# Kernel tuning notes

Measured on AMD Instinct MI355X. Metric: run time of the kernel, lower is better.

Reference implementation:

```python
import jax, jax.numpy as jnp
import numpy as np

B, N, D = 4096, 64, 128
H = 2
M = 3 * D            # model_dim = feat + edge + time
DK = M // H          # d_k = d_v = 192


def setup_inputs() -> dict:
    key = jax.random.key(0)
    ks = jax.random.split(key, 20)
    s = 0.02
    mask = jax.random.randint(ks[6], (B, N), 0, 2).astype(bool)
    mask = mask.at[:, 0].set(False)  # guarantee >=1 valid neighbor per row
    return {
        "src":   jax.random.normal(ks[0], (B, D), jnp.float32),
        "src_t": jax.random.normal(ks[1], (B, 1, D), jnp.float32),
        "src_s": jax.random.normal(ks[2], (B, D), jnp.float32),
        "seq":   jax.random.normal(ks[3], (B, N, D), jnp.float32),
        "seq_t": jax.random.normal(ks[4], (B, N, D), jnp.float32),
        "seq_e": jax.random.normal(ks[5], (B, N, D), jnp.float32),
        "mask":  mask,
        # MapBasedMultiHeadAttention params (torch Linear convention: [out, in])
        "Wq": jax.random.normal(ks[7], (M, M), jnp.float32) * s,
        "Wk": jax.random.normal(ks[8], (M, M), jnp.float32) * s,
        "Wv": jax.random.normal(ks[9], (M, M), jnp.float32) * s,
        "w_map": jax.random.normal(ks[10], (2 * DK,), jnp.float32) * s,
        "Wfc": jax.random.normal(ks[11], (M, M), jnp.float32) * s,
        "bfc": jnp.zeros((M,), jnp.float32),
        "ln_g": jnp.ones((M,), jnp.float32),
        "ln_b": jnp.zeros((M,), jnp.float32),
        # MergeLayer params
        "W1": jax.random.normal(ks[12], (D, M + D), jnp.float32) * s,
        "b1": jnp.zeros((D,), jnp.float32),
        "W2": jax.random.normal(ks[13], (D, D), jnp.float32) * s,
        "b2": jnp.zeros((D,), jnp.float32),
    }


def reference(src, src_t, src_s, seq, seq_t, seq_e, mask,
              Wq, Wk, Wv, w_map, Wfc, bfc, ln_g, ln_b, W1, b1, W2, b2):
    # AttnModel.forward with attn_mode='map', dropout in eval mode.
    q_in = jnp.concatenate([src[:, None, :], src_s[:, None, :], src_t], axis=2)  # [B,1,M]
    k_in = jnp.concatenate([seq, seq_e, seq_t], axis=2)                           # [B,N,M]

    qp = (q_in @ Wq.T).reshape(B, 1, H, DK)   # [B,1,H,dk]
    kp = (k_in @ Wk.T).reshape(B, N, H, DK)   # [B,N,H,dk]
    vp = (k_in @ Wv.T).reshape(B, N, H, DK)   # [B,N,H,dv]

    # weight_map(cat([q,k])) decomposes exactly: w1.q + w2.k (no bias, no nonlinearity before softmax)
    w1, w2 = w_map[:DK], w_map[DK:]
    logit = (jnp.einsum('bqhd,d->bhq', qp, w1)[:, :, :, None]
             + jnp.einsum('bnhd,d->bhn', kp, w2)[:, :, None, :])  # [B,H,1,N]
    logit = jnp.where(mask[:, None, None, :], -1e10, logit)
    attn = jax.nn.softmax(logit, axis=-1)                          # [B,H,1,N]

    out = jnp.einsum('bhqn,bnhd->bqhd', attn, vp).reshape(B, M)    # len_q == 1
    out = jax.nn.leaky_relu(out @ Wfc.T + bfc, negative_slope=0.2)
    out = out + q_in[:, 0, :]                                       # residual
    mu = out.mean(-1, keepdims=True)
    var = ((out - mu) ** 2).mean(-1, keepdims=True)
    out = (out - mu) / jnp.sqrt(var + 1e-5) * ln_g + ln_b           # LayerNorm

    # MergeLayer(output, src)
    x = jnp.concatenate([out, src], axis=1)                         # [B, M+D]
    h = jax.nn.relu(x @ W1.T + b1)
    output = h @ W2.T + b2                                          # [B, D]

    # torch attn after squeeze: [n_head*B, N], head-major
    attn_out = attn[:, :, 0, :].transpose(1, 0, 2).reshape(H * B, N)
    return output, attn_out
```

## Files before the change

### kernel.cpp

```cpp
#include <hip/hip_runtime.h>
#include <hip/hip_bf16.h>

#define B_ 4096
#define N_ 64
#define D_ 128
#define H_ 2
#define M_ 384
#define DK_ 192

#define WS_WKEFF 64
#define WS_W1T   1024
#define WS_W2T   66560
#define WS_WVB   82944
#define WS_WFCB  156672
#define WS_CTXB  230400
#define WS_OUTVB 1803264
#define WS_R     2589696
#define WS_TOTAL 4162560

typedef __attribute__((ext_vector_type(8))) short bf16x8;
typedef __attribute__((ext_vector_type(4))) float f32x4;

__device__ __forceinline__ unsigned short bf1(float a) {
    return __builtin_bit_cast(unsigned short, __float2bfloat16(a));
}

__global__ __launch_bounds__(256) void prep2(
    const float* __restrict__ Wk, const float* __restrict__ wmap,
    const float* __restrict__ W1, const float* __restrict__ W2,
    const float* __restrict__ Wv, const float* __restrict__ Wfc,
    const void* __restrict__ mask, int* __restrict__ flag,
    float* __restrict__ wkeff, float* __restrict__ W1t, float* __restrict__ W2t,
    unsigned short* __restrict__ Wvb, unsigned short* __restrict__ Wfcb) {
    const int tid = threadIdx.x;
    if (blockIdx.x == 0 && tid == 0) {
        const unsigned int* u = (const unsigned int*)mask;
        bool all01 = true, allf = true;
        for (int i = 0; i < 64; ++i) {
            unsigned int v = u[i];
            if (v != 0u && v != 1u) all01 = false;
            if (v != 0u && v != 0x3f800000u) allf = false;
        }
        *flag = all01 ? 0 : (allf ? 2 : 1);
    }
    const int lane = tid & 63, wave = tid >> 6;
    const int gw = blockIdx.x * 4 + wave;
    if (gw < H_ * M_) {
        const int h = gw / M_, m = gw - h * M_;
        float s = 0.f;
        #pragma unroll
        for (int i = 0; i < 3; ++i) {
            int d = lane + i * 64;
            s += wmap[DK_ + d] * Wk[(size_t)(h * DK_ + d) * M_ + m];
        }
        #pragma unroll
        for (int off = 1; off < 64; off <<= 1) s += __shfl_xor(s, off, 64);
        if (lane == 0) wkeff[gw] = s;
    }
    const int gt = blockIdx.x * 256 + tid;
    const int stride = gridDim.x * 256;
    for (int i = gt; i < (M_ + D_) * D_; i += stride) {
        int k = i >> 7, o = i & 127;
        W1t[i] = W1[(size_t)o * (M_ + D_) + k];
    }
    for (int i = gt; i < D_ * D_; i += stride) {
        int k = i >> 7, o = i & 127;
        W2t[i] = W2[(size_t)o * D_ + k];
    }
    for (int i = gt; i < M_ * M_; i += stride) {
        Wvb[i]  = bf1(Wv[i]);
        Wfcb[i] = bf1(Wfc[i]);
    }
}

__global__ __launch_bounds__(256) void attn_v4(
    const float* __restrict__ seq, const float* __restrict__ seqE,
    const float* __restrict__ seqT, const void* __restrict__ mask,
    const float* __restrict__ wkeff, const int* __restrict__ flagp,
    unsigned short* __restrict__ ctxb, float* __restrict__ attn_out) {
    __shared__ float scacc[4][16][50];
    __shared__ float swl[2][64];
    __shared__ float sel[4][2];

    const int b = blockIdx.x;
    const int tid = threadIdx.x;
    const int lane = tid & 63;
    const int wv = tid >> 6;
    const int j8 = tid & 15;
    const int g = tid >> 4;
    const int flag = *flagp;

    float wr0[24], wr1[24];
    #pragma unroll
    for (int t = 0; t < 3; ++t) {
        float4 a0 = *(const float4*)&wkeff[t * 128 + j8 * 8];
        float4 a1 = *(const float4*)&wkeff[t * 128 + j8 * 8 + 4];
        float4 b0 = *(const float4*)&wkeff[M_ + t * 128 + j8 * 8];
        float4 b1 = *(const float4*)&wkeff[M_ + t * 128 + j8 * 8 + 4];
        wr0[t*8+0]=a0.x; wr0[t*8+1]=a0.y; wr0[t*8+2]=a0.z; wr0[t*8+3]=a0.w;
        wr0[t*8+4]=a1.x; wr0[t*8+5]=a1.y; wr0[t*8+6]=a1.z; wr0[t*8+7]=a1.w;
        wr1[t*8+0]=b0.x; wr1[t*8+1]=b0.y; wr1[t*8+2]=b0.z; wr1[t*8+3]=b0.w;
        wr1[t*8+4]=b1.x; wr1[t*8+5]=b1.y; wr1[t*8+6]=b1.z; wr1[t*8+7]=b1.w;
    }

    float cacc0[24], cacc1[24];
    #pragma unroll
    for (int j = 0; j < 24; ++j) { cacc0[j] = 0.f; cacc1[j] = 0.f; }
    float el0 = 0.f, el1 = 0.f;

    const size_t bbase = (size_t)b * (N_ * D_);

    #pragma unroll
    for (int it = 0; it < 4; ++it) {
        const int n = g + (it << 4);
        const size_t off = bbase + (size_t)n * 128 + j8 * 8;
        float v[24];
        {
            float4 va0 = *(const float4*)&seq [off];
            float4 va1 = *(const float4*)&seq [off + 4];
            float4 vb0 = *(const float4*)&seqE[off];
            float4 vb1 = *(const float4*)&seqE[off + 4];
            float4 vc0 = *(const float4*)&seqT[off];
            float4 vc1 = *(const float4*)&seqT[off + 4];
            v[0]=va0.x; v[1]=va0.y; v[2]=va0.z; v[3]=va0.w;
            v[4]=va1.x; v[5]=va1.y; v[6]=va1.z; v[7]=va1.w;
            v[8]=vb0.x; v[9]=vb0.y; v[10]=vb0.z; v[11]=vb0.w;
            v[12]=vb1.x; v[13]=vb1.y; v[14]=vb1.z; v[15]=vb1.w;
            v[16]=vc0.x; v[17]=vc0.y; v[18]=vc0.z; v[19]=vc0.w;
            v[20]=vc1.x; v[21]=vc1.y; v[22]=vc1.z; v[23]=vc1.w;
        }
        float a0 = 0.f, a1 = 0.f;
        #pragma unroll
        for (int j = 0; j < 24; ++j) { a0 += v[j] * wr0[j]; a1 += v[j] * wr1[j]; }
        #pragma unroll
        for (int o = 1; o < 16; o <<= 1) {
            a0 += __shfl_xor(a0, o, 64);
            a1 += __shfl_xor(a1, o, 64);
        }
        int mv;
        if (flag == 0)      mv = ((const int*)mask)[(size_t)b * N_ + n];
        else if (flag == 1) mv = ((const unsigned char*)mask)[(size_t)b * N_ + n];
        else                mv = (((const unsigned int*)mask)[(size_t)b * N_ + n] != 0u) ? 1 : 0;
        float w0, w1;
        if (mv) { w0 = 0.f; w1 = 0.f; }
        else    { w0 = __expf(a0); w1 = __expf(a1); }
        el0 += w0; el1 += w1;
        if (j8 == 0) { swl[0][n] = w0; swl[1][n] = w1; }
        #pragma unroll
        for (int j = 0; j < 24; ++j) { cacc0[j] += w0 * v[j]; cacc1[j] += w1 * v[j]; }
    }

    #pragma unroll
    for (int o = 16; o <= 32; o <<= 1) {
        #pragma unroll
        for (int j = 0; j < 24; ++j) {
            cacc0[j] += __shfl_xor(cacc0[j], o, 64);
            cacc1[j] += __shfl_xor(cacc1[j], o, 64);
        }
    }
    #pragma unroll
    for (int o = 1; o < 64; o <<= 1) {
        el0 += __shfl_xor(el0, o, 64);
        el1 += __shfl_xor(el1, o, 64);
    }
    if (lane < 16) {
        float* dst = &scacc[wv][lane][0];
        #pragma unroll
        for (int j = 0; j < 24; ++j) { dst[j] = cacc0[j]; dst[24 + j] = cacc1[j]; }
    }
    if (lane == 0) { sel[wv][0] = el0; sel[wv][1] = el1; }
    __syncthreads();

    const float l0 = (sel[0][0] + sel[1][0] + sel[2][0] + sel[3][0]) * 0.0625f;
    const float l1 = (sel[0][1] + sel[1][1] + sel[2][1] + sel[3][1]) * 0.0625f;
    const float r0i = 1.f / l0, r1i = 1.f / l1;

    for (int o = tid; o < H_ * M_; o += 256) {
        const int h = (o >= M_) ? 1 : 0;
        const int m = o - h * M_;
        const int t = m >> 7, c = m & 127;
        const int jm = c >> 3, jj = c & 7;
        const int idx = h * 24 + t * 8 + jj;
        float s = scacc[0][jm][idx] + scacc[1][jm][idx] + scacc[2][jm][idx] + scacc[3][jm][idx];
        ctxb[(size_t)b * (H_ * M_) + o] = bf1(s * (h ? r1i : r0i));
    }
    if (tid < H_ * N_) {
        const int h = tid >> 6, n = tid & 63;
        attn_out[((size_t)h * B_ + b) * N_ + n] = swl[h][n] * (h ? r1i : r0i);
    }
}

__global__ __launch_bounds__(256) void gemm_v_mfma(
    const unsigned short* __restrict__ ctxb, const unsigned short* __restrict__ Wvb,
    unsigned short* __restrict__ outvb) {
    const int tid = threadIdx.x;
    const int wave = tid >> 6, lane = tid & 63;
    const int i0 = blockIdx.x * 64;
    const int j0 = blockIdx.y * 64;
    const int aOff = (j0 >= DK_) ? M_ : 0;
    const int r0 = i0 + wave * 16;
    const int lr = lane & 15, lk = (lane >> 4) * 8;
    f32x4 acc[4] = {{0,0,0,0},{0,0,0,0},{0,0,0,0},{0,0,0,0}};
    const unsigned short* arow = &ctxb[(size_t)(r0 + lr) * (H_ * M_) + aOff + lk];
    #pragma unroll
    for (int kk = 0; kk < M_; kk += 32) {
        bf16x8 af = *(const bf16x8*)&arow[kk];
        #pragma unroll
        for (int jn = 0; jn < 4; ++jn) {
            bf16x8 bfr = *(const bf16x8*)&Wvb[(size_t)(j0 + jn * 16 + lr) * M_ + kk + lk];
            acc[jn] = __builtin_amdgcn_mfma_f32_16x16x32_bf16(af, bfr, acc[jn], 0, 0, 0);
        }
    }
    #pragma unroll
    for (int jn = 0; jn < 4; ++jn)
        #pragma unroll
        for (int q = 0; q < 4; ++q) {
            int row = r0 + (lane >> 4) * 4 + q;
            outvb[(size_t)row * M_ + j0 + jn * 16 + lr] = bf1(acc[jn][q]);
        }
}

__global__ __launch_bounds__(256) void gemm_fc_mfma(
    const unsigned short* __restrict__ outvb, const unsigned short* __restrict__ Wfcb,
    const float* __restrict__ bfc,
    const float* __restrict__ src, const float* __restrict__ src_s, const float* __restrict__ src_t,
    float* __restrict__ rws) {
    const int tid = threadIdx.x;
    const int wave = tid >> 6, lane = tid & 63;
    const int i0 = blockIdx.x * 64;
    const int j0 = blockIdx.y * 64;
    const int r0 = i0 + wave * 16;
    const int lr = lane & 15, lk = (lane >> 4) * 8;
    f32x4 acc[4] = {{0,0,0,0},{0,0,0,0},{0,0,0,0},{0,0,0,0}};
    const unsigned short* arow = &outvb[(size_t)(r0 + lr) * M_ + lk];
    #pragma unroll
    for (int kk = 0; kk < M_; kk += 32) {
        bf16x8 af = *(const bf16x8*)&arow[kk];
        #pragma unroll
        for (int jn = 0; jn < 4; ++jn) {
            bf16x8 bfr = *(const bf16x8*)&Wfcb[(size_t)(j0 + jn * 16 + lr) * M_ + kk + lk];
            acc[jn] = __builtin_amdgcn_mfma_f32_16x16x32_bf16(af, bfr, acc[jn], 0, 0, 0);
        }
    }
    const float* qsrc = (j0 < D_) ? src : (j0 < 2 * D_) ? src_s : src_t;
    const int joff = j0 % D_;
    #pragma unroll
    for (int jn = 0; jn < 4; ++jn)
        #pragma unroll
        for (int q = 0; q < 4; ++q) {
            int row = r0 + (lane >> 4) * 4 + q;
            int jc = jn * 16 + lr;
            float t = acc[jn][q] + bfc[j0 + jc];
            t = t > 0.f ? t : 0.2f * t;
            t += qsrc[(size_t)row * D_ + joff + jc];
            rws[(size_t)row * M_ + j0 + jc] = t;
        }
}

__global__ __launch_bounds__(256) void ln_mlp(
    const float* __restrict__ rin, const float* __restrict__ src,
    const float* __restrict__ g, const float* __restrict__ bta,
    const float* __restrict__ W1t, const float* __restrict__ b1,
    const float* __restrict__ W2t, const float* __restrict__ b2,
    float* __restrict__ outp) {
    __shared__ float sa[8 * 520];
    __shared__ float sh[8 * 132];
    const int b0 = blockIdx.x * 8;
    const int tid = threadIdx.x;
    const int row = tid >> 5, part = tid & 31;
    const size_t gr = (size_t)(b0 + row);
    {
        const float* rr = &rin[gr * M_];
        float4 v[3];
        float s = 0.f, sq = 0.f;
        #pragma unroll
        for (int i = 0; i < 3; ++i) {
            v[i] = *(const float4*)&rr[(part + i * 32) * 4];
            s  += v[i].x + v[i].y + v[i].z + v[i].w;
            sq += v[i].x * v[i].x + v[i].y * v[i].y + v[i].z * v[i].z + v[i].w * v[i].w;
        }
        #pragma unroll
        for (int off = 1; off < 32; off <<= 1) {
            s += __shfl_xor(s, off, 64); sq += __shfl_xor(sq, off, 64);
        }
        float mu = s * (1.f / 384.f);
        float rs = rsqrtf(sq * (1.f / 384.f) - mu * mu + 1e-5f);
        #pragma unroll
        for (int i = 0; i < 3; ++i) {
            int k = (part + i * 32) * 4;
            float4 g4 = *(const float4*)&g[k];
            float4 b4 = *(const float4*)&bta[k];
            float4 z;
            z.x = (v[i].x - mu) * rs * g4.x + b4.x;
            z.y = (v[i].y - mu) * rs * g4.y + b4.y;
            z.z = (v[i].z - mu) * rs * g4.z + b4.z;
            z.w = (v[i].w - mu) * rs * g4.w + b4.w;
            *(float4*)&sa[row * 520 + k] = z;
        }
        *(float4*)&sa[row * 520 + M_ + part * 4] = *(const float4*)&src[gr * D_ + part * 4];
    }
    __syncthreads();
    const int c4 = part * 4;
    float acc[4] = {};
    const float* ar = &sa[row * 520];
    #pragma unroll 4
    for (int k4 = 0; k4 < 128; ++k4) {
        float4 a4 = *(const float4*)&ar[k4 * 4];
        #pragma unroll
        for (int j = 0; j < 4; ++j) {
            int k = k4 * 4 + j;
            float a = (j == 0) ? a4.x : (j == 1) ? a4.y : (j == 2) ? a4.z : a4.w;
            float4 w = *(const float4*)&W1t[k * D_ + c4];
            acc[0] += a * w.x; acc[1] += a * w.y; acc[2] += a * w.z; acc[3] += a * w.w;
        }
    }
    {
        float4 bb = *(const float4*)&b1[c4];
        float4 hh;
        hh.x = fmaxf(acc[0] + bb.x, 0.f);
        hh.y = fmaxf(acc[1] + bb.y, 0.f);
        hh.z = fmaxf(acc[2] + bb.z, 0.f);
        hh.w = fmaxf(acc[3] + bb.w, 0.f);
        *(float4*)&sh[row * 132 + c4] = hh;
    }
    __syncthreads();
    float acc2[4] = {};
    const float* hr = &sh[row * 132];
    #pragma unroll 4
    for (int k4 = 0; k4 < 32; ++k4) {
        float4 a4 = *(const float4*)&hr[k4 * 4];
        #pragma unroll
        for (int j = 0; j < 4; ++j) {
            int k = k4 * 4 + j;
            float a = (j == 0) ? a4.x : (j == 1) ? a4.y : (j == 2) ? a4.z : a4.w;
            float4 w = *(const float4*)&W2t[k * D_ + c4];
            acc2[0] += a * w.x; acc2[1] += a * w.y; acc2[2] += a * w.z; acc2[3] += a * w.w;
        }
    }
    float4 bb2 = *(const float4*)&b2[c4];
    float4 oo = make_float4(acc2[0] + bb2.x, acc2[1] + bb2.y, acc2[2] + bb2.z, acc2[3] + bb2.w);
    *(float4*)&outp[gr * D_ + c4] = oo;
}

extern "C" void kernel_launch(void* const* d_in, const int* in_sizes, int n_in,
                              void* d_out, int out_size, void* d_ws, size_t ws_size,
                              hipStream_t stream) {
    (void)in_sizes; (void)n_in; (void)out_size;
    const float* src   = (const float*)d_in[0];
    const float* src_t = (const float*)d_in[1];
    const float* src_s = (const float*)d_in[2];
    const float* seq   = (const float*)d_in[3];
    const float* seq_t = (const float*)d_in[4];
    const float* seq_e = (const float*)d_in[5];
    const void*  mask  = d_in[6];
    const float* Wk    = (const float*)d_in[8];
    const float* Wv    = (const float*)d_in[9];
    const float* wmap  = (const float*)d_in[10];
    const float* Wfc   = (const float*)d_in[11];
    const float* bfc   = (const float*)d_in[12];
    const float* ln_g  = (const float*)d_in[13];
    const float* ln_b  = (const float*)d_in[14];
    const float* W1    = (const float*)d_in[15];
    const float* b1    = (const float*)d_in[16];
    const float* W2    = (const float*)d_in[17];
    const float* b2    = (const float*)d_in[18];

    if (ws_size < (size_t)WS_TOTAL * sizeof(float)) return;
    float* wsf   = (float*)d_ws;
    int*   flagp = (int*)d_ws;
    float* wkeff = wsf + WS_WKEFF;
    float* W1t   = wsf + WS_W1T;
    float* W2t   = wsf + WS_W2T;
    unsigned short* Wvb   = (unsigned short*)(wsf + WS_WVB);
    unsigned short* Wfcb  = (unsigned short*)(wsf + WS_WFCB);
    unsigned short* ctxb  = (unsigned short*)(wsf + WS_CTXB);
    unsigned short* outvb = (unsigned short*)(wsf + WS_OUTVB);
    float* rws   = wsf + WS_R;
    float* outp     = (float*)d_out;
    float* attn_out = outp + (size_t)B_ * D_;

    prep2<<<256, 256, 0, stream>>>(Wk, wmap, W1, W2, Wv, Wfc, mask, flagp,
                                   wkeff, W1t, W2t, Wvb, Wfcb);
    attn_v4<<<B_, 256, 0, stream>>>(seq, seq_e, seq_t, mask, wkeff, flagp, ctxb, attn_out);
    gemm_v_mfma<<<dim3(64, 6), 256, 0, stream>>>(ctxb, Wvb, outvb);
    gemm_fc_mfma<<<dim3(64, 6), 256, 0, stream>>>(outvb, Wfcb, bfc, src, src_s, src_t, rws);
    ln_mlp<<<512, 256, 0, stream>>>(rws, src, ln_g, ln_b, W1t, b1, W2t, b2, outp);
}
```

Baseline: 172.5 us.

## Fuse V and FC GEMMs via LDS; split attention launch with nontemporal loads

The two back-to-back MFMA GEMMs (ctx·Wv and outv·Wfc) become one kernel. Each 256-thread block handles 16 rows and keeps the intermediate bf16 tile in shared memory, so the global round trip through outvb is gone. The attention kernel is templated and launched twice over the two halves of the batch. The first half uses nontemporal loads for seq/seq_e/seq_t, probably so that streamed data does not evict L2 lines the second half or the GEMM could reuse. As a trade-off, the fused GEMM runs with only 256 blocks, each doing more work, so occupancy and weight reuse per block change.

```diff
diff --git a/kernel.cpp b/kernel.cpp
--- a/kernel.cpp
+++ b/kernel.cpp
@@ -14,7 +14,6 @@
 #define WS_WVB   82944
 #define WS_WFCB  156672
 #define WS_CTXB  230400
-#define WS_OUTVB 1803264
 #define WS_R     2589696
 #define WS_TOTAL 4162560
 
@@ -73,16 +72,26 @@
     }
 }
 
-__global__ __launch_bounds__(256) void attn_v4(
+template <bool NT>
+__device__ __forceinline__ float4 ld4(const float* p) {
+    if (NT) {
+        f32x4 r = __builtin_nontemporal_load((const f32x4*)p);
+        return *(float4*)&r;
+    }
+    return *(const float4*)p;
+}
+
+template <bool NT>
+__global__ __launch_bounds__(256) void attn_v4k(
     const float* __restrict__ seq, const float* __restrict__ seqE,
     const float* __restrict__ seqT, const void* __restrict__ mask,
     const float* __restrict__ wkeff, const int* __restrict__ flagp,
-    unsigned short* __restrict__ ctxb, float* __restrict__ attn_out) {
+    unsigned short* __restrict__ ctxb, float* __restrict__ attn_out, int b0off) {
     __shared__ float scacc[4][16][50];
     __shared__ float swl[2][64];
     __shared__ float sel[4][2];
 
-    const int b = blockIdx.x;
+    const int b = blockIdx.x + b0off;
     const int tid = threadIdx.x;
     const int lane = tid & 63;
     const int wv = tid >> 6;
@@ -116,12 +125,12 @@
         const size_t off = bbase + (size_t)n * 128 + j8 * 8;
         float v[24];
         {
-            float4 va0 = *(const float4*)&seq [off];
-            float4 va1 = *(const float4*)&seq [off + 4];
-            float4 vb0 = *(const float4*)&seqE[off];
-            float4 vb1 = *(const float4*)&seqE[off + 4];
-            float4 vc0 = *(const float4*)&seqT[off];
-            float4 vc1 = *(const float4*)&seqT[off + 4];
+            float4 va0 = ld4<NT>(&seq [off]);
+            float4 va1 = ld4<NT>(&seq [off + 4]);
+            float4 vb0 = ld4<NT>(&seqE[off]);
+            float4 vb1 = ld4<NT>(&seqE[off + 4]);
+            float4 vc0 = ld4<NT>(&seqT[off]);
+            float4 vc1 = ld4<NT>(&seqT[off + 4]);
             v[0]=va0.x; v[1]=va0.y; v[2]=va0.z; v[3]=va0.w;
             v[4]=va1.x; v[5]=va1.y; v[6]=va1.z; v[7]=va1.w;
             v[8]=vb0.x; v[9]=vb0.y; v[10]=vb0.z; v[11]=vb0.w;
@@ -190,71 +199,67 @@
     }
 }
 
-__global__ __launch_bounds__(256) void gemm_v_mfma(
+#define SOUTSTRIDE 392
+__global__ __launch_bounds__(256) void gemm_vfc(
     const unsigned short* __restrict__ ctxb, const unsigned short* __restrict__ Wvb,
-    unsigned short* __restrict__ outvb) {
+    const unsigned short* __restrict__ Wfcb, const float* __restrict__ bfc,
+    const float* __restrict__ src, const float* __restrict__ src_s, const float* __restrict__ src_t,
+    float* __restrict__ rws) {
+    __shared__ __hip_bfloat16 sout[16 * SOUTSTRIDE];
     const int tid = threadIdx.x;
     const int wave = tid >> 6, lane = tid & 63;
-    const int i0 = blockIdx.x * 64;
-    const int j0 = blockIdx.y * 64;
-    const int aOff = (j0 >= DK_) ? M_ : 0;
-    const int r0 = i0 + wave * 16;
+    const int r0 = blockIdx.x * 16;
     const int lr = lane & 15, lk = (lane >> 4) * 8;
-    f32x4 acc[4] = {{0,0,0,0},{0,0,0,0},{0,0,0,0},{0,0,0,0}};
+    const int aOff = (wave >= 2) ? M_ : 0;
+
+    f32x4 acc[6] = {};
     const unsigned short* arow = &ctxb[(size_t)(r0 + lr) * (H_ * M_) + aOff + lk];
     #pragma unroll
     for (int kk = 0; kk < M_; kk += 32) {
         bf16x8 af = *(const bf16x8*)&arow[kk];
         #pragma unroll
-        for (int jn = 0; jn < 4; ++jn) {
-            bf16x8 bfr = *(const bf16x8*)&Wvb[(size_t)(j0 + jn * 16 + lr) * M_ + kk + lk];
-            acc[jn] = __builtin_amdgcn_mfma_f32_16x16x32_bf16(af, bfr, acc[jn], 0, 0, 0);
-        }
-    }
-    #pragma unroll
-    for (int jn = 0; jn < 4; ++jn)
+        for (int jt = 0; jt < 6; ++jt) {
+            const int j0 = wave * 96 + jt * 16;
+            bf16x8 bfr = *(const bf16x8*)&Wvb[(size_t)(j0 + lr) * M_ + kk + lk];
+            acc[jt] = __builtin_amdgcn_mfma_f32_16x16x32_bf16(af, bfr, acc[jt], 0, 0, 0);
+        }
+    }
+    #pragma unroll
+    for (int jt = 0; jt < 6; ++jt)
         #pragma unroll
         for (int q = 0; q < 4; ++q) {
-            int row = r0 + (lane >> 4) * 4 + q;
-            outvb[(size_t)row * M_ + j0 + jn * 16 + lr] = bf1(acc[jn][q]);
-        }
-}
-
-__global__ __launch_bounds__(256) void gemm_fc_mfma(
-    const unsigned short* __restrict__ outvb, const unsigned short* __restrict__ Wfcb,
-    const float* __restrict__ bfc,
-    const float* __restrict__ src, const float* __restrict__ src_s, const float* __restrict__ src_t,
-    float* __restrict__ rws) {
-    const int tid = threadIdx.x;
-    const int wave = tid >> 6, lane = tid & 63;
-    const int i0 = blockIdx.x * 64;
-    const int j0 = blockIdx.y * 64;
-    const int r0 = i0 + wave * 16;
-    const int lr = lane & 15, lk = (lane >> 4) * 8;
-    f32x4 acc[4] = {{0,0,0,0},{0,0,0,0},{0,0,0,0},{0,0,0,0}};
-    const unsigned short* arow = &outvb[(size_t)(r0 + lr) * M_ + lk];
+            const int row = (lane >> 4) * 4 + q;
+            sout[row * SOUTSTRIDE + wave * 96 + jt * 16 + lr] =
+                __float2bfloat16(acc[jt][q]);
+        }
+    __syncthreads();
+
+    f32x4 acc2[6] = {};
     #pragma unroll
     for (int kk = 0; kk < M_; kk += 32) {
-        bf16x8 af = *(const bf16x8*)&arow[kk];
-        #pragma unroll
-        for (int jn = 0; jn < 4; ++jn) {
-            bf16x8 bfr = *(const bf16x8*)&Wfcb[(size_t)(j0 + jn * 16 + lr) * M_ + kk + lk];
-            acc[jn] = __builtin_amdgcn_mfma_f32_16x16x32_bf16(af, bfr, acc[jn], 0, 0, 0);
-        }
-    }
-    const float* qsrc = (j0 < D_) ? src : (j0 < 2 * D_) ? src_s : src_t;
-    const int joff = j0 % D_;
-    #pragma unroll
-    for (int jn = 0; jn < 4; ++jn)
+        bf16x8 af = *(const bf16x8*)&sout[lr * SOUTSTRIDE + kk + lk];
+        #pragma unroll
+        for (int jt = 0; jt < 6; ++jt) {
+            const int j0 = wave * 96 + jt * 16;
+            bf16x8 bfr = *(const bf16x8*)&Wfcb[(size_t)(j0 + lr) * M_ + kk + lk];
+            acc2[jt] = __builtin_amdgcn_mfma_f32_16x16x32_bf16(af, bfr, acc2[jt], 0, 0, 0);
+        }
+    }
+    #pragma unroll
+    for (int jt = 0; jt < 6; ++jt) {
+        const int j0 = wave * 96 + jt * 16;
+        const float* qsrc = (j0 < D_) ? src : (j0 < 2 * D_) ? src_s : src_t;
+        const int joff = j0 - ((j0 < D_) ? 0 : (j0 < 2 * D_) ? D_ : 2 * D_);
         #pragma unroll
         for (int q = 0; q < 4; ++q) {
-            int row = r0 + (lane >> 4) * 4 + q;
-            int jc = jn * 16 + lr;
-            float t = acc[jn][q] + bfc[j0 + jc];
+            const int row = r0 + (lane >> 4) * 4 + q;
+            const int jc = j0 + lr;
+            float t = acc2[jt][q] + bfc[jc];
             t = t > 0.f ? t : 0.2f * t;
-            t += qsrc[(size_t)row * D_ + joff + jc];
-            rws[(size_t)row * M_ + j0 + jc] = t;
-        }
+            t += qsrc[(size_t)row * D_ + joff + lr];
+            rws[(size_t)row * M_ + jc] = t;
+        }
+    }
 }
 
 __global__ __launch_bounds__(256) void ln_mlp(
@@ -374,15 +379,16 @@
     unsigned short* Wvb   = (unsigned short*)(wsf + WS_WVB);
     unsigned short* Wfcb  = (unsigned short*)(wsf + WS_WFCB);
     unsigned short* ctxb  = (unsigned short*)(wsf + WS_CTXB);
-    unsigned short* outvb = (unsigned short*)(wsf + WS_OUTVB);
     float* rws   = wsf + WS_R;
     float* outp     = (float*)d_out;
     float* attn_out = outp + (size_t)B_ * D_;
 
     prep2<<<256, 256, 0, stream>>>(Wk, wmap, W1, W2, Wv, Wfc, mask, flagp,
                                    wkeff, W1t, W2t, Wvb, Wfcb);
-    attn_v4<<<B_, 256, 0, stream>>>(seq, seq_e, seq_t, mask, wkeff, flagp, ctxb, attn_out);
-    gemm_v_mfma<<<dim3(64, 6), 256, 0, stream>>>(ctxb, Wvb, outvb);
-    gemm_fc_mfma<<<dim3(64, 6), 256, 0, stream>>>(outvb, Wfcb, bfc, src, src_s, src_t, rws);
+    attn_v4k<true><<<B_ / 2, 256, 0, stream>>>(seq, seq_e, seq_t, mask, wkeff, flagp,
+                                               ctxb, attn_out, 0);
+    attn_v4k<false><<<B_ / 2, 256, 0, stream>>>(seq, seq_e, seq_t, mask, wkeff, flagp,
+                                                ctxb, attn_out, B_ / 2);
+    gemm_vfc<<<256, 256, 0, stream>>>(ctxb, Wvb, Wfcb, bfc, src, src_s, src_t, rws);
     ln_mlp<<<512, 256, 0, stream>>>(rws, src, ln_g, ln_b, W1t, b1, W2t, b2, outp);
 }
```

After: 154.1 us. 10.7% less time.
